# Optimization experiments

Hardware: AMD Instinct MI355X
Metric: run time of the kernel (lower is better)

The kernel has to match this reference:

```python
import jax, jax.numpy as jnp
import numpy as np

DIM = 512
HEADS = 8
ALPHA = 0.5
HIDDEN = int(DIM * 2.0)
EPS = 1e-5


def _layernorm(x, g, b):
    mu = jnp.mean(x, axis=-1, keepdims=True)
    var = jnp.var(x, axis=-1, keepdims=True)
    return (x - mu) * jax.lax.rsqrt(var + EPS) * g + b


def setup_inputs() -> dict:
    key = jax.random.key(0)
    ks = jax.random.split(key, 8)
    B, N, C = 4, 1536, DIM
    s = lambda fan_in: 1.0 / np.sqrt(fan_in)
    return {
        "x": jax.random.normal(ks[0], (B, N, C), dtype=jnp.float32),
        "ln1_g": jnp.ones((C,), jnp.float32),
        "ln1_b": jnp.zeros((C,), jnp.float32),
        "qkv_w": jax.random.normal(ks[1], (C, 3 * C), jnp.float32) * s(C),
        "qkv_b": jnp.zeros((3 * C,), jnp.float32),
        "ln2_g": jnp.ones((C,), jnp.float32),
        "ln2_b": jnp.zeros((C,), jnp.float32),
        "fc1_w": jax.random.normal(ks[2], (C, HIDDEN), jnp.float32) * s(C),
        "fc1_b": jnp.zeros((HIDDEN,), jnp.float32),
        "fc2_w": jax.random.normal(ks[3], (HIDDEN, C), jnp.float32) * s(HIDDEN),
        "fc2_b": jnp.zeros((C,), jnp.float32),
    }


def reference(x, ln1_g, ln1_b, qkv_w, qkv_b, ln2_g, ln2_b, fc1_w, fc1_b, fc2_w, fc2_b):
    B, N, C = x.shape
    H = HEADS
    d = C // H
    S = N // 3

    h = _layernorm(x, ln1_g, ln1_b)
    qkv = (h @ qkv_w + qkv_b).reshape(B, N, 3, H, d)
    qkv = jnp.transpose(qkv, (2, 0, 3, 1, 4))  # [3,B,H,N,d]
    q, k, v = qkv[0], qkv[1], qkv[2]

    attn = jnp.einsum('bhnd,bhmd->bhnm', q, k) * (d ** -0.5)  # [B,H,N,N]
    # sequential cross-segment score mixing (matches in-place torch semantics)
    s0 = attn[:, :, 0:S]
    s1 = attn[:, :, S:2 * S] + ALPHA * s0
    s2 = attn[:, :, 2 * S:] + ALPHA * s1
    attn = jnp.concatenate([s0, s1, s2], axis=2)
    attn = jax.nn.softmax(attn, axis=-1)

    o = jnp.einsum('bhnm,bhmd->bhnd', attn, v)
    o = jnp.transpose(o, (0, 2, 1, 3)).reshape(B, N, C)
    x = x + o  # NOTE: self.proj is defined but unused in the original forward

    h2 = _layernorm(x, ln2_g, ln2_b)
    m = jax.nn.gelu(h2 @ fc1_w + fc1_b, approximate=False) @ fc2_w + fc2_b
    return x + m
```

## Files before the change

kernel.cpp:

```cpp
#include <hip/hip_runtime.h>
#include <hip/hip_bf16.h>
#include <math.h>

#define DIMC 512
#define NSEQ 1536
#define BATCH 4
#define NHEADS 8
#define HDIM 64
#define SSEG 512
#define HIDDEN_DIM 1024
#define ALPHA_C 0.5f
#define EPS_C 1e-5f
#define NROWS (BATCH*NSEQ)
#define SHIFT_L2 8.65617025f
#define QSCALE_L2 0.18033688f

typedef __attribute__((ext_vector_type(8))) short bfrag8;
typedef __attribute__((ext_vector_type(8))) _Float16 hfrag8;
typedef __attribute__((ext_vector_type(2))) __fp16 h2;
typedef __attribute__((ext_vector_type(4))) float ffrag;
typedef float4 f4;


__device__ __forceinline__ ushort f2bf(float v) {
    __hip_bfloat16 hb = __float2bfloat16(v);
    return *(ushort*)&hb;
}

__device__ __forceinline__ void gl2lds16(const ushort* g, ushort* l) {
    __builtin_amdgcn_global_load_lds(
        (const __attribute__((address_space(1))) unsigned*)g,
        (__attribute__((address_space(3))) unsigned*)l, 16, 0, 0);
}

__global__ __launch_bounds__(256)
void prep_kernel(const float* __restrict__ qkv_w, const float* __restrict__ fc1_w,
                 const float* __restrict__ fc2_w, ushort* __restrict__ qkv_wt,
                 ushort* __restrict__ fc1_wt, ushort* __restrict__ fc2_wt,
                 const float* __restrict__ x, const float* __restrict__ g,
                 const float* __restrict__ bvec, ushort* __restrict__ h_out)
{
    int bid = blockIdx.x;
    if (bid < 448) {
        __shared__ float tile[64][65];
        const float* W; ushort* Wt; int K, N, n0, k0;
        if (bid < 192)      { W = qkv_w; Wt = qkv_wt; K = 512;  N = 1536; int b = bid;       n0 = (b % 24) * 64; k0 = (b / 24) * 64; }
        else if (bid < 320) { W = fc1_w; Wt = fc1_wt; K = 512;  N = 1024; int b = bid - 192; n0 = (b % 16) * 64; k0 = (b / 16) * 64; }
        else                { W = fc2_w; Wt = fc2_wt; K = 1024; N = 512;  int b = bid - 320; n0 = (b % 8)  * 64; k0 = (b / 8)  * 64; }
        int tx = threadIdx.x & 63, ty = threadIdx.x >> 6;
        #pragma unroll
        for (int i = 0; i < 16; i++) {
            int r = i * 4 + ty;
            tile[r][tx] = W[(size_t)(k0 + r) * N + n0 + tx];
        }
        __syncthreads();
        #pragma unroll
        for (int i = 0; i < 16; i++) {
            int r = i * 4 + ty;
            Wt[(size_t)(n0 + r) * K + k0 + tx] = f2bf(tile[tx][r]);
        }
    } else {
        __shared__ float red[16];
        int row = bid - 448;
        int t = threadIdx.x;
        int lane = t & 63, w = t >> 6;
        const float* rp = x + (size_t)row * DIMC;
        float v0 = rp[t];
        float v1 = rp[t + 256];
        float s = v0 + v1;
        float s2 = v0 * v0 + v1 * v1;
        #pragma unroll
        for (int o = 32; o > 0; o >>= 1) {
            s  += __shfl_down(s,  o, 64);
            s2 += __shfl_down(s2, o, 64);
        }
        if (lane == 0) { red[w] = s; red[8 + w] = s2; }
        __syncthreads();
        if (t == 0) {
            float a = red[0] + red[1] + red[2] + red[3];
            float c = red[8] + red[9] + red[10] + red[11];
            red[0] = a; red[8] = c;
        }
        __syncthreads();
        float mean = red[0] * (1.0f / DIMC);
        float var  = red[8] * (1.0f / DIMC) - mean * mean;
        float rstd = rsqrtf(var + EPS_C);
        ushort* op = h_out + (size_t)row * DIMC;
        op[t]       = f2bf((v0 - mean) * rstd * g[t]       + bvec[t]);
        op[t + 256] = f2bf((v1 - mean) * rstd * g[t + 256] + bvec[t + 256]);
    }
}

__global__ __launch_bounds__(256)
void ln_kernel(const float* __restrict__ in, const float* __restrict__ g,
               const float* __restrict__ b, ushort* __restrict__ out)
{
    __shared__ float red[16];
    int row = blockIdx.x;
    int t = threadIdx.x;
    int lane = t & 63, w = t >> 6;
    const float* rp = in + (size_t)row * DIMC;
    float v0 = rp[t];
    float v1 = rp[t + 256];
    float s = v0 + v1;
    float s2 = v0 * v0 + v1 * v1;
    #pragma unroll
    for (int o = 32; o > 0; o >>= 1) {
        s  += __shfl_down(s,  o, 64);
        s2 += __shfl_down(s2, o, 64);
    }
    if (lane == 0) { red[w] = s; red[8 + w] = s2; }
    __syncthreads();
    if (t == 0) {
        float a = red[0] + red[1] + red[2] + red[3];
        float c = red[8] + red[9] + red[10] + red[11];
        red[0] = a; red[8] = c;
    }
    __syncthreads();
    float mean = red[0] * (1.0f / DIMC);
    float var  = red[8] * (1.0f / DIMC) - mean * mean;
    float rstd = rsqrtf(var + EPS_C);
    ushort* op = out + (size_t)row * DIMC;
    op[t]       = f2bf((v0 - mean) * rstd * g[t]       + b[t]);
    op[t + 256] = f2bf((v1 - mean) * rstd * g[t + 256] + b[t + 256]);
}

template <int EPI>
__device__ __forceinline__
void mgemm_body(const ushort* __restrict__ A, const ushort* __restrict__ Wt,
                const float* __restrict__ bias, const float* resid,
                void* out, int M, int K, int Nn, int bx, int by,
                ushort* As, ushort* Bs)
{
    int tid = threadIdx.x;
    int lane = tid & 63, w = tid >> 6;
    int cl = lane & 15, qg = lane >> 4;
    int wm = w >> 1, wn = w & 1;
    int rowBase = by * 64, colBase = bx * 64;
    int sr = lane >> 2;
    int sb = (lane & 3) * 8;

    const ushort* agb = A  + (size_t)(rowBase + w * 16 + sr) * K + sb;
    const ushort* bgb = Wt + (size_t)(colBase + w * 16 + sr) * K + sb;

    ffrag acc[2][2];
    #pragma unroll
    for (int mi = 0; mi < 2; mi++)
        #pragma unroll
        for (int ni = 0; ni < 2; ni++)
            #pragma unroll
            for (int r = 0; r < 4; r++) acc[mi][ni][r] = 0.f;

    int niter = K >> 6;

    #pragma unroll
    for (int hf = 0; hf < 2; hf++) {
        gl2lds16(agb + hf * 32, As + (0 * 2 + hf) * 2048 + (w * 16) * 32);
        gl2lds16(bgb + hf * 32, Bs + (0 * 2 + hf) * 2048 + (w * 16) * 32);
    }
    __syncthreads();

    for (int it = 0; it < niter; it++) {
        int cur = it & 1;
        if (it + 1 < niter) {
            int k0 = (it + 1) * 64;
            #pragma unroll
            for (int hf = 0; hf < 2; hf++) {
                gl2lds16(agb + k0 + hf * 32, As + ((cur ^ 1) * 2 + hf) * 2048 + (w * 16) * 32);
                gl2lds16(bgb + k0 + hf * 32, Bs + ((cur ^ 1) * 2 + hf) * 2048 + (w * 16) * 32);
            }
        }
        #pragma unroll
        for (int ks = 0; ks < 2; ks++) {
            bfrag8 af[2], bf[2];
            #pragma unroll
            for (int mi = 0; mi < 2; mi++)
                af[mi] = *(const bfrag8*)&As[(cur * 2 + ks) * 2048 + (wm * 32 + mi * 16 + cl) * 32 + qg * 8];
            #pragma unroll
            for (int ni = 0; ni < 2; ni++)
                bf[ni] = *(const bfrag8*)&Bs[(cur * 2 + ks) * 2048 + (wn * 32 + ni * 16 + cl) * 32 + qg * 8];
            #pragma unroll
            for (int mi = 0; mi < 2; mi++)
                #pragma unroll
                for (int ni = 0; ni < 2; ni++)
                    acc[mi][ni] = __builtin_amdgcn_mfma_f32_16x16x32_bf16(af[mi], bf[ni], acc[mi][ni], 0, 0, 0);
        }
        if (it + 1 < niter) __syncthreads();
    }

    int bb = (EPI == 3) ? (colBase / 1536) : 0;

    #pragma unroll
    for (int mi = 0; mi < 2; mi++) {
        #pragma unroll
        for (int ni = 0; ni < 2; ni++) {
            #pragma unroll
            for (int r = 0; r < 4; r++) {
                int row = rowBase + wm * 32 + mi * 16 + qg * 4 + r;
                int col = colBase + wn * 32 + ni * 16 + cl;
                float v = acc[mi][ni][r] + (EPI == 3 ? bias[row] : bias[col]);
                if (EPI == 0 && col < DIMC) v *= QSCALE_L2;
                if (EPI == 1) v = 0.5f * v * (1.0f + erff(v * 0.70710678118654752f));
                if (EPI == 2) {
                    v += resid[(size_t)row * Nn + col];
                    ((float*)out)[(size_t)row * Nn + col] = v;
                } else if (EPI == 3) {
                    int t = col - bb * 1536;
                    int h = row >> 6, dl = row & 63;
                    int t32 = t & 31;
                    int slot = ((t32 & 15) >> 2) * 8 + (t32 >> 4) * 4 + (t32 & 3);
                    size_t a = ((size_t)(bb * 8 + h) * 48 + (t >> 5)) * 2048
                             + (dl >> 4) * 512 + (dl & 15) * 32 + slot;
                    _Float16 e = (_Float16)v;
                    ((ushort*)out)[a] = *(ushort*)&e;
                } else {
                    ((ushort*)out)[(size_t)row * Nn + col] = f2bf(v);
                }
            }
        }
    }
}

template <int EPI>
__device__ __forceinline__
void mgemm128_body(const ushort* __restrict__ A, const ushort* __restrict__ Wt,
                   const float* __restrict__ bias, void* out, void* out2,
                   int K, int Nn, int bx, int by,
                   ushort* As, ushort* Bs)
{
    int tid = threadIdx.x;
    int lane = tid & 63, w = tid >> 6;
    int cl = lane & 15, qg = lane >> 4;
    int wm = w >> 1, wn = w & 1;
    int rowBase = by * 64, colBase = bx * 128;
    int sr = lane >> 2;
    int sb = (lane & 3) * 8;

    const ushort* agb = A  + (size_t)(rowBase + w * 16 + sr) * K + sb;
    const ushort* bgb = Wt + (size_t)(colBase + w * 32 + sr) * K + sb;

    ffrag acc[2][4];
    #pragma unroll
    for (int mi = 0; mi < 2; mi++)
        #pragma unroll
        for (int ni = 0; ni < 4; ni++)
            #pragma unroll
            for (int r = 0; r < 4; r++) acc[mi][ni][r] = 0.f;

    int niter = K >> 6;

    #pragma unroll
    for (int hf = 0; hf < 2; hf++) {
        gl2lds16(agb + hf * 32,                  As + (0 * 2 + hf) * 2048 + (w * 16) * 32);
        gl2lds16(bgb + hf * 32,                  Bs + (0 * 2 + hf) * 4096 + (w * 32) * 32);
        gl2lds16(bgb + (size_t)16 * K + hf * 32, Bs + (0 * 2 + hf) * 4096 + (w * 32 + 16) * 32);
    }
    __syncthreads();

    for (int it = 0; it < niter; it++) {
        int cur = it & 1;
        if (it + 1 < niter) {
            int k0 = (it + 1) * 64;
            #pragma unroll
            for (int hf = 0; hf < 2; hf++) {
                gl2lds16(agb + k0 + hf * 32,                  As + ((cur ^ 1) * 2 + hf) * 2048 + (w * 16) * 32);
                gl2lds16(bgb + k0 + hf * 32,                  Bs + ((cur ^ 1) * 2 + hf) * 4096 + (w * 32) * 32);
                gl2lds16(bgb + (size_t)16 * K + k0 + hf * 32, Bs + ((cur ^ 1) * 2 + hf) * 4096 + (w * 32 + 16) * 32);
            }
        }
        #pragma unroll
        for (int ks = 0; ks < 2; ks++) {
            bfrag8 af[2], bf[4];
            #pragma unroll
            for (int mi = 0; mi < 2; mi++)
                af[mi] = *(const bfrag8*)&As[(cur * 2 + ks) * 2048 + (wm * 32 + mi * 16 + cl) * 32 + qg * 8];
            #pragma unroll
            for (int ni = 0; ni < 4; ni++)
                bf[ni] = *(const bfrag8*)&Bs[(cur * 2 + ks) * 4096 + (wn * 64 + ni * 16 + cl) * 32 + qg * 8];
            #pragma unroll
            for (int mi = 0; mi < 2; mi++)
                #pragma unroll
                for (int ni = 0; ni < 4; ni++)
                    acc[mi][ni] = __builtin_amdgcn_mfma_f32_16x16x32_bf16(af[mi], bf[ni], acc[mi][ni], 0, 0, 0);
        }
        if (it + 1 < niter) __syncthreads();
    }

    int bb = (EPI == 4) ? (rowBase / 1536) : 0;

    #pragma unroll
    for (int mi = 0; mi < 2; mi++) {
        #pragma unroll
        for (int ni = 0; ni < 4; ni++) {
            #pragma unroll
            for (int r = 0; r < 4; r++) {
                int row = rowBase + wm * 32 + mi * 16 + qg * 4 + r;
                int col = colBase + wn * 64 + ni * 16 + cl;
                float v = acc[mi][ni][r] + bias[col];
                if (EPI == 1) {
                    v = 0.5f * v * (1.0f + erff(v * 0.70710678118654752f));
                    ((ushort*)out)[(size_t)row * Nn + col] = f2bf(v);
                } else if (EPI == 4) {
                    int t = row - bb * 1536;
                    int h = (col >> 6) & 7;
                    int d = col & 63;
                    size_t a = ((size_t)(bb * 8 + h) * 96 + (t >> 4)) * 1024
                             + (d >> 5) * 512 + (t & 15) * 32 + (d & 31);
                    if (col < DIMC) {
                        v *= QSCALE_L2;
                        ((ushort*)out)[a] = f2bf(v);
                    } else {
                        ((ushort*)out2)[a] = f2bf(v);
                    }
                }
            }
        }
    }
}

template <int EPI>
__global__ __launch_bounds__(256)
void mgemm_kernel(const ushort* __restrict__ A, const ushort* __restrict__ Wt,
                  const float* __restrict__ bias, const float* resid,
                  void* out, int M, int K, int Nn)
{
    __shared__ ushort As[2 * 2 * 64 * 32];
    __shared__ ushort Bs[2 * 2 * 64 * 32];
    mgemm_body<EPI>(A, Wt, bias, resid, out, M, K, Nn, blockIdx.x, blockIdx.y, As, Bs);
}

template <int EPI>
__global__ __launch_bounds__(256)
void mgemm128_kernel(const ushort* __restrict__ A, const ushort* __restrict__ Wt,
                     const float* __restrict__ bias, void* out, int K, int Nn)
{
    __shared__ ushort As[2 * 2 * 64 * 32];
    __shared__ ushort Bs[2 * 2 * 128 * 32];
    mgemm128_body<EPI>(A, Wt, bias, out, nullptr, K, Nn, blockIdx.x, blockIdx.y, As, Bs);
}

__global__ __launch_bounds__(256)
void qkvt_kernel(const ushort* __restrict__ h_bf, const ushort* __restrict__ qkv_wt,
                 const float* __restrict__ qkv_b, ushort* __restrict__ qpk,
                 ushort* __restrict__ kpk, ushort* __restrict__ vpk)
{
    __shared__ ushort smem[2 * 2 * 192 * 32];
    int bid = blockIdx.x;
    if (bid < 768) {
        mgemm128_body<4>(h_bf, qkv_wt, qkv_b, (void*)qpk, (void*)kpk,
                         DIMC, 2 * DIMC, bid & 7, bid >> 3,
                         smem, smem + 2 * 2 * 64 * 32);
    } else {
        int b2 = bid - 768;
        mgemm_body<3>(qkv_wt + (size_t)2 * DIMC * DIMC, h_bf, qkv_b + 2 * DIMC, nullptr,
                      (void*)vpk, DIMC, DIMC, NROWS, b2 % 96, b2 / 96,
                      smem, smem + 2 * 2 * 64 * 32);
    }
}

__global__ __launch_bounds__(256)
void attn_kernel(const ushort* __restrict__ qpk, const ushort* __restrict__ kpk,
                 const ushort* __restrict__ vpk,
                 const float* __restrict__ x, float* __restrict__ xres)
{
    __shared__ float Op[48][68];
    __shared__ float Lp[4][4][16][3];

    int n = blockIdx.x + (blockIdx.y << 5);
    int idx = n >> 3;
    int bh  = (n & 7) * 4 + (idx & 3);
    int qi0 = (idx >> 2) * 16;
    int b = bh >> 3, h = bh & 7;
    int tid = threadIdx.x;
    int lane = tid & 63, w = tid >> 6;
    int cl = lane & 15, qg = lane >> 4;

    int lofs = cl * 32 + qg * 8;
    const ushort* qb = qpk + (size_t)bh * 96 * 1024;
    const ushort* kb = kpk + (size_t)bh * 96 * 1024;
    const ushort* vb = vpk + (size_t)bh * 48 * 2048;

    bfrag8 bq[3][2];
    #pragma unroll
    for (int seg = 0; seg < 3; seg++)
        #pragma unroll
        for (int f = 0; f < 2; f++)
            bq[seg][f] = *(const bfrag8*)&qb[(size_t)((seg * SSEG + qi0) >> 4) * 1024 + f * 512 + lofs];

    ffrag o[3][4];
    #pragma unroll
    for (int seg = 0; seg < 3; seg++)
        #pragma unroll
        for (int mg = 0; mg < 4; mg++)
            #pragma unroll
            for (int r = 0; r < 4; r++) o[seg][mg][r] = 0.f;
    float lp[3] = {0.f, 0.f, 0.f};

    int kb0 = w * 384;

    const ushort* kptr = kb + (size_t)(kb0 >> 4) * 1024 + lofs;
    const ushort* vptr = vb + (size_t)(kb0 >> 5) * 2048 + lofs;

    auto loadf = [&](hfrag8* av, bfrag8 (*af)[2]) {
        #pragma unroll
        for (int mg = 0; mg < 4; mg++)
            av[mg] = *(const hfrag8*)(vptr + mg * 512);
        vptr += 2048;
        #pragma unroll
        for (int s = 0; s < 2; s++)
            #pragma unroll
            for (int f = 0; f < 2; f++)
                af[s][f] = *(const bfrag8*)(kptr + s * 1024 + f * 512);
        kptr += 2048;
    };

    auto comp = [&](const hfrag8* av, const bfrag8 (*af)[2]) {
        ffrag c[2][3];
        #pragma unroll
        for (int s = 0; s < 2; s++) {
            #pragma unroll
            for (int seg = 0; seg < 3; seg++) {
                #pragma unroll
                for (int r = 0; r < 4; r++) c[s][seg][r] = 0.f;
                c[s][seg] = __builtin_amdgcn_mfma_f32_16x16x32_bf16(af[s][0], bq[seg][0], c[s][seg], 0, 0, 0);
                c[s][seg] = __builtin_amdgcn_mfma_f32_16x16x32_bf16(af[s][1], bq[seg][1], c[s][seg], 0, 0, 0);
            }
        }
        #pragma unroll
        for (int s = 0; s < 2; s++) {
            #pragma unroll
            for (int r = 0; r < 4; r++) {
                float s0 = c[s][0][r];
                float s1 = c[s][1][r] + ALPHA_C * s0;
                float s2 = c[s][2][r] + ALPHA_C * s1;
                float e0 = __builtin_amdgcn_exp2f(s0 - SHIFT_L2);
                float e1 = __builtin_amdgcn_exp2f(s1 - SHIFT_L2);
                float e2 = __builtin_amdgcn_exp2f(s2 - SHIFT_L2);
                c[s][0][r] = e0; c[s][1][r] = e1; c[s][2][r] = e2;
                lp[0] += e0; lp[1] += e1; lp[2] += e2;
            }
        }
        #pragma unroll
        for (int seg = 0; seg < 3; seg++) {
            union { hfrag8 v8; h2 v2[4]; } u;
            u.v2[0] = __builtin_amdgcn_cvt_pkrtz(c[0][seg][0], c[0][seg][1]);
            u.v2[1] = __builtin_amdgcn_cvt_pkrtz(c[0][seg][2], c[0][seg][3]);
            u.v2[2] = __builtin_amdgcn_cvt_pkrtz(c[1][seg][0], c[1][seg][1]);
            u.v2[3] = __builtin_amdgcn_cvt_pkrtz(c[1][seg][2], c[1][seg][3]);
            #pragma unroll
            for (int mg = 0; mg < 4; mg++)
                o[seg][mg] = __builtin_amdgcn_mfma_f32_16x16x32_f16(av[mg], u.v8, o[seg][mg], 0, 0, 0);
        }
    };

    hfrag8 avA[4], avB[4];
    bfrag8 afA[2][2], afB[2][2];
    loadf(avA, afA);
    #pragma unroll 1
    for (int it = 0; it < 12; it += 2) {
        loadf(avB, afB);
        comp(avA, afA);
        if (it + 2 < 12) loadf(avA, afA);
        comp(avB, afB);
    }

    #pragma unroll
    for (int seg = 0; seg < 3; seg++) Lp[w][qg][cl][seg] = lp[seg];

    #pragma unroll 1
    for (int wv = 0; wv < 4; wv++) {
        __syncthreads();
        if (w == wv) {
            #pragma unroll
            for (int seg = 0; seg < 3; seg++)
                #pragma unroll
                for (int mg = 0; mg < 4; mg++) {
                    float* dst = &Op[seg * 16 + cl][mg * 16 + qg * 4];
                    if (wv == 0) {
                        #pragma unroll
                        for (int r = 0; r < 4; r++) dst[r] = o[seg][mg][r];
                    } else {
                        #pragma unroll
                        for (int r = 0; r < 4; r++) dst[r] += o[seg][mg][r];
                    }
                }
        }
    }
    __syncthreads();

    if (tid < 192) {
        int row = tid >> 2;
        int seg = row >> 4, q16 = row & 15;
        int d0 = (tid & 3) * 16;
        float l = 0.f;
        #pragma unroll
        for (int wv = 0; wv < 4; wv++)
            #pragma unroll
            for (int g2 = 0; g2 < 4; g2++)
                l += Lp[wv][g2][q16][seg];
        float invl = 1.0f / l;
        size_t rowg = ((size_t)(b * NSEQ + seg * SSEG + qi0 + q16)) * DIMC + h * HDIM + d0;
        #pragma unroll
        for (int dd = 0; dd < 16; dd += 4) {
            f4 xv = *(const f4*)(x + rowg + dd);
            f4 ov;
            ov.x = Op[row][d0 + dd + 0] * invl + xv.x;
            ov.y = Op[row][d0 + dd + 1] * invl + xv.y;
            ov.z = Op[row][d0 + dd + 2] * invl + xv.z;
            ov.w = Op[row][d0 + dd + 3] * invl + xv.w;
            *(f4*)(xres + rowg + dd) = ov;
        }
    }
}

extern "C" void kernel_launch(void* const* d_in, const int* in_sizes, int n_in,
                              void* d_out, int out_size, void* d_ws, size_t ws_size,
                              hipStream_t stream)
{
    const float* x     = (const float*)d_in[0];
    const float* ln1_g = (const float*)d_in[1];
    const float* ln1_b = (const float*)d_in[2];
    const float* qkv_w = (const float*)d_in[3];
    const float* qkv_b = (const float*)d_in[4];
    const float* ln2_g = (const float*)d_in[5];
    const float* ln2_b = (const float*)d_in[6];
    const float* fc1_w = (const float*)d_in[7];
    const float* fc1_b = (const float*)d_in[8];
    const float* fc2_w = (const float*)d_in[9];
    const float* fc2_b = (const float*)d_in[10];
    float* out = (float*)d_out;

    char* p = (char*)d_ws;
    ushort* h_bf    = (ushort*)p;  p += (size_t)NROWS * DIMC * 2;
    ushort* qpk     = (ushort*)p;  p += (size_t)32 * 96 * 1024 * 2;
    ushort* kpk     = (ushort*)p;  p += (size_t)32 * 96 * 1024 * 2;
    ushort* vpk     = (ushort*)p;  p += (size_t)32 * 48 * 2048 * 2;
    ushort* mid     = (ushort*)p;  p += (size_t)NROWS * HIDDEN_DIM * 2;
    ushort* qkv_wt  = (ushort*)p;  p += (size_t)3 * DIMC * DIMC * 2;
    ushort* fc1_wt  = (ushort*)p;  p += (size_t)HIDDEN_DIM * DIMC * 2;
    ushort* fc2_wt  = (ushort*)p;
    float* xres = out;

    prep_kernel<<<448 + NROWS, 256, 0, stream>>>(qkv_w, fc1_w, fc2_w, qkv_wt, fc1_wt, fc2_wt,
                                                 x, ln1_g, ln1_b, h_bf);

    qkvt_kernel<<<1536, 256, 0, stream>>>(h_bf, qkv_wt, qkv_b, qpk, kpk, vpk);

    attn_kernel<<<dim3(SSEG / 16, BATCH * NHEADS), 256, 0, stream>>>(qpk, kpk, vpk, x, xres);

    ln_kernel<<<NROWS, 256, 0, stream>>>(xres, ln2_g, ln2_b, h_bf);

    mgemm128_kernel<1><<<dim3(HIDDEN_DIM / 128, NROWS / 64), 256, 0, stream>>>(
        h_bf, fc1_wt, fc1_b, (void*)mid, DIMC, HIDDEN_DIM);

    mgemm_kernel<2><<<dim3(DIMC / 64, NROWS / 64), 256, 0, stream>>>(
        mid, fc2_wt, fc2_b, xres, (void*)out, NROWS, HIDDEN_DIM, DIMC);
}
```

Measured before the change: 191.3 us.

## Fold softmax shift into MFMA init and compute row sums via MFMA

```diff
diff --git a/kernel.cpp b/kernel.cpp
--- a/kernel.cpp
+++ b/kernel.cpp
@@ -13,6 +13,7 @@
 #define EPS_C 1e-5f
 #define NROWS (BATCH*NSEQ)
 #define SHIFT_L2 8.65617025f
+#define HSHIFT_L2 4.328085125f
 #define QSCALE_L2 0.18033688f
 
 typedef __attribute__((ext_vector_type(8))) short bfrag8;
@@ -394,7 +395,15 @@
         for (int mg = 0; mg < 4; mg++)
             #pragma unroll
             for (int r = 0; r < 4; r++) o[seg][mg][r] = 0.f;
-    float lp[3] = {0.f, 0.f, 0.f};
+    ffrag ol[3];
+    #pragma unroll
+    for (int seg = 0; seg < 3; seg++)
+        #pragma unroll
+        for (int r = 0; r < 4; r++) ol[seg][r] = 0.f;
+
+    hfrag8 vq;
+    #pragma unroll
+    for (int j = 0; j < 8; j++) vq[j] = (_Float16)0.25f;
 
     int kb0 = w * 384;
 
@@ -417,27 +426,32 @@
     auto comp = [&](const hfrag8* av, const bfrag8 (*af)[2]) {
         ffrag c[2][3];
         #pragma unroll
-        for (int s = 0; s < 2; s++) {
+        for (int s = 0; s < 2; s++)
+            #pragma unroll
+            for (int r = 0; r < 4; r++) {
+                c[s][0][r] = -SHIFT_L2;
+                c[s][1][r] = -HSHIFT_L2;
+                c[s][2][r] = -HSHIFT_L2;
+            }
+        __builtin_amdgcn_s_setprio(1);
+        #pragma unroll
+        for (int s = 0; s < 2; s++)
             #pragma unroll
             for (int seg = 0; seg < 3; seg++) {
-                #pragma unroll
-                for (int r = 0; r < 4; r++) c[s][seg][r] = 0.f;
                 c[s][seg] = __builtin_amdgcn_mfma_f32_16x16x32_bf16(af[s][0], bq[seg][0], c[s][seg], 0, 0, 0);
                 c[s][seg] = __builtin_amdgcn_mfma_f32_16x16x32_bf16(af[s][1], bq[seg][1], c[s][seg], 0, 0, 0);
             }
-        }
+        __builtin_amdgcn_s_setprio(0);
         #pragma unroll
         for (int s = 0; s < 2; s++) {
             #pragma unroll
             for (int r = 0; r < 4; r++) {
-                float s0 = c[s][0][r];
-                float s1 = c[s][1][r] + ALPHA_C * s0;
-                float s2 = c[s][2][r] + ALPHA_C * s1;
-                float e0 = __builtin_amdgcn_exp2f(s0 - SHIFT_L2);
-                float e1 = __builtin_amdgcn_exp2f(s1 - SHIFT_L2);
-                float e2 = __builtin_amdgcn_exp2f(s2 - SHIFT_L2);
-                c[s][0][r] = e0; c[s][1][r] = e1; c[s][2][r] = e2;
-                lp[0] += e0; lp[1] += e1; lp[2] += e2;
+                float sh0 = c[s][0][r];
+                float sh1 = fmaf(ALPHA_C, sh0, c[s][1][r]);
+                float sh2 = fmaf(ALPHA_C, sh1, c[s][2][r]);
+                c[s][0][r] = __builtin_amdgcn_exp2f(sh0);
+                c[s][1][r] = __builtin_amdgcn_exp2f(sh1);
+                c[s][2][r] = __builtin_amdgcn_exp2f(sh2);
             }
         }
         #pragma unroll
@@ -447,9 +461,12 @@
             u.v2[1] = __builtin_amdgcn_cvt_pkrtz(c[0][seg][2], c[0][seg][3]);
             u.v2[2] = __builtin_amdgcn_cvt_pkrtz(c[1][seg][0], c[1][seg][1]);
             u.v2[3] = __builtin_amdgcn_cvt_pkrtz(c[1][seg][2], c[1][seg][3]);
+            __builtin_amdgcn_s_setprio(1);
             #pragma unroll
             for (int mg = 0; mg < 4; mg++)
                 o[seg][mg] = __builtin_amdgcn_mfma_f32_16x16x32_f16(av[mg], u.v8, o[seg][mg], 0, 0, 0);
+            ol[seg] = __builtin_amdgcn_mfma_f32_16x16x32_f16(vq, u.v8, ol[seg], 0, 0, 0);
+            __builtin_amdgcn_s_setprio(0);
         }
     };
 
@@ -465,7 +482,7 @@
     }
 
     #pragma unroll
-    for (int seg = 0; seg < 3; seg++) Lp[w][qg][cl][seg] = lp[seg];
+    for (int seg = 0; seg < 3; seg++) Lp[w][qg][cl][seg] = ol[seg][0];
 
     #pragma unroll 1
     for (int wv = 0; wv < 4; wv++) {
```

Result: slower. 208.5 us (+9.0%).
